# Performance work log

Measured on AMD Instinct MI355X. Metric: run time of the kernel, lower is better.

## Reference

```python
import jax, jax.numpy as jnp
from jax import lax
import numpy as np

VOCAB, EMB = 50000, 300
HID, NCLS = 100, 20
BATCH, SEQ = 128, 512
P_DROP = 0.5


def setup_inputs() -> dict:
    key = jax.random.key(0)
    ks = jax.random.split(key, 8)
    s_e = 1.0 / np.sqrt(EMB)
    s_h = 1.0 / np.sqrt(HID)
    return {
        "inputs_batch": jax.random.randint(ks[0], (BATCH, SEQ), 0, VOCAB, dtype=jnp.int64)
        if jax.config.jax_enable_x64 else jax.random.randint(ks[0], (BATCH, SEQ), 0, VOCAB, dtype=jnp.int32),
        "emb_table": jax.random.normal(ks[1], (VOCAB, EMB), dtype=jnp.float32),
        # GRUCell params (torch layout): gates order [r, z, n]
        "w_ih": jax.random.uniform(ks[2], (3 * HID, EMB), jnp.float32, -s_h, s_h),
        "w_hh": jax.random.uniform(ks[3], (3 * HID, HID), jnp.float32, -s_h, s_h),
        "b_ih": jax.random.uniform(ks[4], (3 * HID,), jnp.float32, -s_h, s_h),
        "b_hh": jax.random.uniform(ks[5], (3 * HID,), jnp.float32, -s_h, s_h),
        "w_lin": jax.random.uniform(ks[6], (NCLS, HID), jnp.float32, -s_h, s_h),
        "b_lin": jax.random.uniform(ks[7], (NCLS,), jnp.float32, -s_h, s_h),
    }


def reference(inputs_batch, emb_table, w_ih, w_hh, b_ih, b_hh, w_lin, b_lin):
    B, S = inputs_batch.shape
    H = w_hh.shape[1]
    keep = 1.0 - P_DROP
    dk1, dk2 = jax.random.split(jax.random.key(42))

    z_embed = emb_table[inputs_batch]                       # [B, S, E]
    m1 = jax.random.bernoulli(dk1, keep, z_embed.shape)     # dropout1 mask
    z_embed = jnp.where(m1, z_embed / keep, 0.0)
    x_seq = jnp.swapaxes(z_embed, 0, 1)                     # [S, B, E]
    m2 = jax.random.bernoulli(dk2, keep, (S, B, H))         # per-step dropout2 masks

    def step(h, inp):
        x, m = inp
        gi = x @ w_ih.T + b_ih                              # [B, 3H]
        gh = h @ w_hh.T + b_hh
        i_r, i_z, i_n = jnp.split(gi, 3, axis=-1)
        h_r, h_z, h_n = jnp.split(gh, 3, axis=-1)
        r = jax.nn.sigmoid(i_r + h_r)
        zg = jax.nn.sigmoid(i_z + h_z)
        n = jnp.tanh(i_n + r * h_n)
        h_new = (1.0 - zg) * n + zg * h
        h_d = jnp.where(m, h_new / keep, 0.0)
        y = jax.nn.log_softmax(h_d @ w_lin.T + b_lin, axis=1)  # [B, C]
        return h_new, y

    h0 = jnp.zeros((B, H), dtype=x_seq.dtype)
    _, ys = lax.scan(step, h0, (x_seq, m2))                 # ys: [S, B, C]
    return jnp.transpose(ys, (1, 2, 0))                     # [B, C, S]
```

## Files before the change

### kernel.cpp

```cpp
#include <hip/hip_runtime.h>
#include <hip/hip_bf16.h>
#include <cstdint>

#define BATCH 128
#define SEQ   512
#define EMB   300
#define HID   100
#define G3    300
#define NCLS  20
#define NROWS (SEQ * BATCH)

#define M1_WORDS 614400
#define M2_WORDS 204800

typedef __attribute__((ext_vector_type(4))) float f32x4;
typedef __attribute__((ext_vector_type(8))) short s16x8;
typedef __fp16 h16x2 __attribute__((ext_vector_type(2)));

__host__ __device__ __forceinline__ void threefry2x32(uint32_t k0, uint32_t k1,
                                                      uint32_t x0, uint32_t x1,
                                                      uint32_t* o0, uint32_t* o1) {
  uint32_t ks2 = k0 ^ k1 ^ 0x1BD11BDAu;
  x0 += k0; x1 += k1;
#define TFR(r) { x0 += x1; x1 = (x1 << (r)) | (x1 >> (32 - (r))); x1 ^= x0; }
  TFR(13) TFR(15) TFR(26) TFR(6)  x0 += k1;  x1 += ks2 + 1u;
  TFR(17) TFR(29) TFR(16) TFR(24) x0 += ks2; x1 += k0 + 2u;
  TFR(13) TFR(15) TFR(26) TFR(6)  x0 += k0;  x1 += k1 + 3u;
  TFR(17) TFR(29) TFR(16) TFR(24) x0 += k1;  x1 += ks2 + 4u;
  TFR(13) TFR(15) TFR(26) TFR(6)  x0 += ks2; x1 += k0 + 5u;
#undef TFR
  *o0 = x0; *o1 = x1;
}

__device__ __forceinline__ uint32_t rand_bits32(uint32_t ka, uint32_t kb, uint32_t flat) {
  uint32_t a, b;
  threefry2x32(ka, kb, 0u, flat, &a, &b);
  return a ^ b;
}

__device__ __forceinline__ short f2bf(float f) {
  union { float f; uint32_t u; } c; c.f = f;
  uint32_t u = c.u;
  return (short)((u + 0x7FFFu + ((u >> 16) & 1u)) >> 16);
}

__device__ __forceinline__ void bar_lds() {
  __asm__ __volatile__("s_waitcnt lgkmcnt(0)" ::: "memory");
  __builtin_amdgcn_s_barrier();
  __asm__ __volatile__("" ::: "memory");
}

__global__ __launch_bounds__(256) void k_mask(uint32_t* __restrict__ M1w,
                                              uint32_t* __restrict__ M2w,
                                              uint32_t k1a, uint32_t k1b,
                                              uint32_t k2a, uint32_t k2b) {
  const int i = blockIdx.x * 256 + threadIdx.x;
  uint32_t ka, kb, base;
  uint32_t* dst;
  if (i < M1_WORDS) { ka = k1a; kb = k1b; base = (uint32_t)i * 32u; dst = M1w + i; }
  else { ka = k2a; kb = k2b; base = (uint32_t)(i - M1_WORDS) * 32u; dst = M2w + (i - M1_WORDS); }
  uint32_t w = 0u;
#pragma unroll
  for (int j = 0; j < 32; ++j) {
    uint32_t bits = rand_bits32(ka, kb, base + (uint32_t)j);
    w |= ((~bits) >> 31) << j;
  }
  *dst = w;
}

__global__ __launch_bounds__(256) void k_prepw(const float* __restrict__ w_ih,
                                               short* __restrict__ Wb) {
  int i8 = (blockIdx.x * 256 + threadIdx.x) * 8;
  if (i8 >= 304 * 320) return;
  short o[8];
#pragma unroll
  for (int j = 0; j < 8; ++j) {
    int pos = i8 + j;
    int n = pos / 320, k = pos - (pos / 320) * 320;
    float v = (n < 300 && k < 300) ? w_ih[(size_t)n * EMB + k] : 0.f;
    o[j] = f2bf(v);
  }
  *(s16x8*)(Wb + i8) = *(s16x8*)o;
}

__global__ __launch_bounds__(512) void k_gi7(const int* __restrict__ inputs,
                                             const float* __restrict__ emb,
                                             const short* __restrict__ Wb,
                                             const float* __restrict__ b_ih,
                                             const uint32_t* __restrict__ M1w,
                                             float* __restrict__ GI) {
  __shared__ short As[128 * 40];
  __shared__ short Bs[304 * 40];
  __shared__ int idxs[128];
  const int t = threadIdx.x;
  const int s = blockIdx.x;
  const int lane = t & 63, wave = t >> 6;
  const int wr = wave & 1;
  const int wc = wave >> 1;
  const int ml = lane & 15, quad = lane >> 4;
  const int arow = t >> 2;
  const int akq = t & 3;

  if (t < 128) idxs[t] = inputs[t * SEQ + s];
  __syncthreads();

  const int nfr = (wc < 3) ? 5 : 4;
  f32x4 acc[4][5];
#pragma unroll
  for (int i = 0; i < 4; ++i)
#pragma unroll
    for (int j = 0; j < 5; ++j) acc[i][j] = (f32x4){0.f, 0.f, 0.f, 0.f};

  const int myidx = idxs[arow];

  for (int c = 0; c < 10; ++c) {
    const int e0 = c * 32 + akq * 8;
    float xa[8];
#pragma unroll
    for (int j = 0; j < 8; ++j) xa[j] = 0.f;
    if (e0 + 7 < 300) {
#pragma unroll
      for (int q4 = 0; q4 < 2; ++q4) {
        float4 v = *(const float4*)(emb + (size_t)myidx * EMB + e0 + q4 * 4);
        xa[q4 * 4 + 0] = v.x; xa[q4 * 4 + 1] = v.y; xa[q4 * 4 + 2] = v.z; xa[q4 * 4 + 3] = v.w;
      }
    } else if (e0 < 300) {
#pragma unroll
      for (int j = 0; j < 8; ++j) {
        int e = e0 + j;
        if (e < 300) xa[j] = emb[(size_t)myidx * EMB + e];
      }
    }
    uint32_t mb = 0;
    if (e0 < 300) {
      uint32_t base = (uint32_t)((arow * SEQ + s) * EMB + e0);
      uint64_t mw = (uint64_t)M1w[base >> 5] | ((uint64_t)M1w[(base >> 5) + 1] << 32);
      mb = (uint32_t)(mw >> (base & 31));
    }
    short sa[8];
#pragma unroll
    for (int j = 0; j < 8; ++j)
      sa[j] = f2bf(((mb >> j) & 1u) ? xa[j] * 2.f : 0.f);
    s16x8 bv0, bv1, bv2;
    {
      int i0 = t;
      bv0 = *(const s16x8*)(Wb + (size_t)(i0 >> 2) * 320 + c * 32 + (i0 & 3) * 8);
      int i1 = t + 512;
      bv1 = *(const s16x8*)(Wb + (size_t)(i1 >> 2) * 320 + c * 32 + (i1 & 3) * 8);
      if (t < 192) {
        int i2 = t + 1024;
        bv2 = *(const s16x8*)(Wb + (size_t)(i2 >> 2) * 320 + c * 32 + (i2 & 3) * 8);
      }
    }
    if (c > 0) __syncthreads();
    *(s16x8*)&As[arow * 40 + akq * 8] = *(s16x8*)&sa[0];
    {
      int i0 = t;       *(s16x8*)&Bs[(i0 >> 2) * 40 + (i0 & 3) * 8] = bv0;
      int i1 = t + 512; *(s16x8*)&Bs[(i1 >> 2) * 40 + (i1 & 3) * 8] = bv1;
      if (t < 192) { int i2 = t + 1024; *(s16x8*)&Bs[(i2 >> 2) * 40 + (i2 & 3) * 8] = bv2; }
    }
    __syncthreads();
    s16x8 af[4];
#pragma unroll
    for (int mt = 0; mt < 4; ++mt)
      af[mt] = *(const s16x8*)&As[(wr * 64 + mt * 16 + ml) * 40 + quad * 8];
#pragma unroll
    for (int j = 0; j < 5; ++j) {
      if (j < nfr) {
        int nt = wc + 4 * j;
        s16x8 bf = *(const s16x8*)&Bs[(nt * 16 + ml) * 40 + quad * 8];
#pragma unroll
        for (int mt = 0; mt < 4; ++mt)
          acc[mt][j] = __builtin_amdgcn_mfma_f32_16x16x32_bf16(af[mt], bf, acc[mt][j], 0, 0, 0);
      }
    }
  }

#pragma unroll
  for (int j = 0; j < 5; ++j) {
    if (j < nfr) {
      int n = (wc + 4 * j) * 16 + ml;
      if (n < 300) {
        float bias = b_ih[n];
#pragma unroll
        for (int mt = 0; mt < 4; ++mt) {
#pragma unroll
          for (int i = 0; i < 4; ++i) {
            int brow = wr * 64 + mt * 16 + quad * 4 + i;
            GI[(size_t)(s * BATCH + brow) * G3 + n] = acc[mt][j][i] + bias;
          }
        }
      }
    }
  }
}

__global__ __launch_bounds__(512, 1) void k_rnn10(const float* __restrict__ GI,
                                                  const float* __restrict__ w_hh,
                                                  const float* __restrict__ b_hh,
                                                  const uint8_t* __restrict__ M2,
                                                  float* __restrict__ Hd) {
  __shared__ float4 part[4][104];
  __shared__ __align__(8) float h_s[100];
  const int t = threadIdx.x, lane = t & 63, wave = t >> 6;
  const int q = wave >> 1, g = wave & 1;
  const int b = blockIdx.x;
  const int ulo = (lane < 36) ? lane : 35;
  const int u = g ? (64 + ulo) : lane;
  const bool dotstore = (g == 0) || (lane < 36);
  const int kplo = (q < 2) ? q * 13 : 26 + (q - 2) * 12;

  const float* rowR = w_hh + (size_t)u * HID;
  const float* rowZ = w_hh + (size_t)(u + 100) * HID;
  const float* rowN = w_hh + (size_t)(u + 200) * HID;
  const int o12 = (kplo + 12 < 50) ? 2 * (kplo + 12) : 96;
#define PK(row, off) __builtin_amdgcn_cvt_pkrtz((row)[off], (row)[(off) + 1])
  const h16x2 wr0 = PK(rowR, 2 * kplo + 0),  wr1 = PK(rowR, 2 * kplo + 2),
              wr2 = PK(rowR, 2 * kplo + 4),  wr3 = PK(rowR, 2 * kplo + 6),
              wr4 = PK(rowR, 2 * kplo + 8),  wr5 = PK(rowR, 2 * kplo + 10),
              wr6 = PK(rowR, 2 * kplo + 12), wr7 = PK(rowR, 2 * kplo + 14),
              wr8 = PK(rowR, 2 * kplo + 16), wr9 = PK(rowR, 2 * kplo + 18),
              wr10 = PK(rowR, 2 * kplo + 20), wr11 = PK(rowR, 2 * kplo + 22),
              wr12 = PK(rowR, o12);
  const h16x2 wz0 = PK(rowZ, 2 * kplo + 0),  wz1 = PK(rowZ, 2 * kplo + 2),
              wz2 = PK(rowZ, 2 * kplo + 4),  wz3 = PK(rowZ, 2 * kplo + 6),
              wz4 = PK(rowZ, 2 * kplo + 8),  wz5 = PK(rowZ, 2 * kplo + 10),
              wz6 = PK(rowZ, 2 * kplo + 12), wz7 = PK(rowZ, 2 * kplo + 14),
              wz8 = PK(rowZ, 2 * kplo + 16), wz9 = PK(rowZ, 2 * kplo + 18),
              wz10 = PK(rowZ, 2 * kplo + 20), wz11 = PK(rowZ, 2 * kplo + 22),
              wz12 = PK(rowZ, o12);
  const h16x2 wn0 = PK(rowN, 2 * kplo + 0),  wn1 = PK(rowN, 2 * kplo + 2),
              wn2 = PK(rowN, 2 * kplo + 4),  wn3 = PK(rowN, 2 * kplo + 6),
              wn4 = PK(rowN, 2 * kplo + 8),  wn5 = PK(rowN, 2 * kplo + 10),
              wn6 = PK(rowN, 2 * kplo + 12), wn7 = PK(rowN, 2 * kplo + 14),
              wn8 = PK(rowN, 2 * kplo + 16), wn9 = PK(rowN, 2 * kplo + 18),
              wn10 = PK(rowN, 2 * kplo + 20), wn11 = PK(rowN, 2 * kplo + 22),
              wn12 = PK(rowN, o12);
#undef PK

  const bool ew = (wave < 4) && (lane < 25);
  const int ue = wave * 25 + lane;
  float bR = 0.f, bZ = 0.f, bN = 0.f, gcR = 0.f, gcZ = 0.f, gcN = 0.f;
  uint8_t mc = 0;
  if (ew) {
    bR = b_hh[ue]; bZ = b_hh[100 + ue]; bN = b_hh[200 + ue];
    const float* g0 = GI + (size_t)b * G3;
    gcR = g0[ue]; gcZ = g0[100 + ue]; gcN = g0[200 + ue];
    mc = M2[(uint32_t)(b * HID + ue) >> 3];
  }

  if (t < 100) h_s[t] = 0.f;
  h16x2 hP = (h16x2){(__fp16)0.f, (__fp16)0.f};
  const int pl = (lane < 50) ? lane : 49;
  __syncthreads();

#define RLP(L) __builtin_bit_cast(h16x2, __builtin_amdgcn_readlane(__builtin_bit_cast(int, hP), (L)))
#define S1P(J, L) { h16x2 hh = RLP(L); \
    sR = __builtin_amdgcn_fdot2(wr##J, hh, sR, false); \
    sZ = __builtin_amdgcn_fdot2(wz##J, hh, sZ, false); \
    sN = __builtin_amdgcn_fdot2(wn##J, hh, sN, false); }
#define DOT12(L0) \
  S1P(0, (L0) + 0)  S1P(1, (L0) + 1)  S1P(2, (L0) + 2)  S1P(3, (L0) + 3)  \
  S1P(4, (L0) + 4)  S1P(5, (L0) + 5)  S1P(6, (L0) + 6)  S1P(7, (L0) + 7)  \
  S1P(8, (L0) + 8)  S1P(9, (L0) + 9)  S1P(10, (L0) + 10) S1P(11, (L0) + 11)
#define DOT13(L0) DOT12(L0) S1P(12, (L0) + 12)

  for (int s = 0; s < SEQ; ++s) {
    float gnR = 0.f, gnZ = 0.f, gnN = 0.f;
    uint8_t mn = 0;
    if (ew) {
      int sn = (s + 1 < SEQ) ? s + 1 : s;
      const float* gp = GI + (size_t)(sn * BATCH + b) * G3;
      gnR = gp[ue]; gnZ = gp[100 + ue]; gnN = gp[200 + ue];
      mn = M2[(uint32_t)((sn * BATCH + b) * HID + ue) >> 3];
    }

    float sR = 0.f, sZ = 0.f, sN = 0.f;
    switch (q) {
      case 0: { DOT13(0)  } break;
      case 1: { DOT13(13) } break;
      case 2: { DOT12(26) } break;
      case 3: { DOT12(38) } break;
    }
    if (dotstore) part[q][u] = make_float4(sR, sZ, sN, 0.f);
    bar_lds();

    if (wave < 4) {
      if (lane < 25) {
        float4 p0 = part[0][ue], p1 = part[1][ue], p2 = part[2][ue], p3 = part[3][ue];
        float hr = (p0.x + p1.x) + (p2.x + p3.x) + bR;
        float hz = (p0.y + p1.y) + (p2.y + p3.y) + bZ;
        float hn = (p0.z + p1.z) + (p2.z + p3.z) + bN;
        float r = 1.f / (1.f + __expf(-(gcR + hr)));
        float z = 1.f / (1.f + __expf(-(gcZ + hz)));
        float xn = gcN + r * hn;
        float e2 = __expf(2.f * fabsf(xn));
        float n = copysignf(1.f - 2.f / (e2 + 1.f), xn);
        float hprev = h_s[ue];
        float hnew = (1.f - z) * n + z * hprev;
        uint32_t fl = (uint32_t)((s * BATCH + b) * HID + ue);
        float hd = ((mc >> (fl & 7)) & 1) ? hnew * 2.f : 0.f;
        Hd[(size_t)(b * SEQ + s) * HID + ue] = hd;
        h_s[ue] = hnew;
      }
    }
    bar_lds();
    {
      float2 hp2 = *(const float2*)&h_s[2 * pl];
      hP = __builtin_amdgcn_cvt_pkrtz(hp2.x, hp2.y);
    }
    gcR = gnR; gcZ = gnZ; gcN = gnN; mc = mn;
  }
#undef DOT13
#undef DOT12
#undef S1P
#undef RLP
}

__global__ __launch_bounds__(64) void k_out(const float* __restrict__ Hd,
                                            const float* __restrict__ w_lin,
                                            const float* __restrict__ b_lin,
                                            float* __restrict__ out) {
  __shared__ float Wl[NCLS * HID];
  __shared__ float bl[NCLS];
  const int t = threadIdx.x;
  for (int i = t; i < NCLS * HID; i += 64) Wl[i] = w_lin[i];
  if (t < NCLS) bl[t] = b_lin[t];
  __syncthreads();

  const int r0 = (blockIdx.x * 64 + t) * 4;
  float acc[4][NCLS];
#pragma unroll
  for (int r = 0; r < 4; ++r)
#pragma unroll
    for (int c = 0; c < NCLS; ++c) acc[r][c] = bl[c];

  for (int k = 0; k < HID; k += 4) {
    float4 h0 = *(const float4*)(Hd + (size_t)(r0 + 0) * HID + k);
    float4 h1 = *(const float4*)(Hd + (size_t)(r0 + 1) * HID + k);
    float4 h2 = *(const float4*)(Hd + (size_t)(r0 + 2) * HID + k);
    float4 h3 = *(const float4*)(Hd + (size_t)(r0 + 3) * HID + k);
#pragma unroll
    for (int c = 0; c < NCLS; ++c) {
      float4 w4 = *(const float4*)&Wl[c * HID + k];
      acc[0][c] += h0.x * w4.x + h0.y * w4.y + h0.z * w4.z + h0.w * w4.w;
      acc[1][c] += h1.x * w4.x + h1.y * w4.y + h1.z * w4.z + h1.w * w4.w;
      acc[2][c] += h2.x * w4.x + h2.y * w4.y + h2.z * w4.z + h2.w * w4.w;
      acc[3][c] += h3.x * w4.x + h3.y * w4.y + h3.z * w4.z + h3.w * w4.w;
    }
  }

  float lse[4];
#pragma unroll
  for (int r = 0; r < 4; ++r) {
    float mx = acc[r][0];
#pragma unroll
    for (int c = 1; c < NCLS; ++c) mx = fmaxf(mx, acc[r][c]);
    float se = 0.f;
#pragma unroll
    for (int c = 0; c < NCLS; ++c) se += __expf(acc[r][c] - mx);
    lse[r] = mx + __logf(se);
  }
  const int b = r0 >> 9, s0 = r0 & 511;
#pragma unroll
  for (int c = 0; c < NCLS; ++c) {
    float4 o = make_float4(acc[0][c] - lse[0], acc[1][c] - lse[1],
                           acc[2][c] - lse[2], acc[3][c] - lse[3]);
    *(float4*)(out + (size_t)(b * NCLS + c) * SEQ + s0) = o;
  }
}

extern "C" void kernel_launch(void* const* d_in, const int* in_sizes, int n_in,
                              void* d_out, int out_size, void* d_ws, size_t ws_size,
                              hipStream_t stream) {
  const int*   inputs = (const int*)d_in[0];
  const float* emb    = (const float*)d_in[1];
  const float* w_ih   = (const float*)d_in[2];
  const float* w_hh   = (const float*)d_in[3];
  const float* b_ih   = (const float*)d_in[4];
  const float* b_hh   = (const float*)d_in[5];
  const float* w_lin  = (const float*)d_in[6];
  const float* b_lin  = (const float*)d_in[7];
  float* out = (float*)d_out;

  float* GI = (float*)d_ws;
  float* Hd = GI + (size_t)NROWS * G3;
  uint8_t* M1 = (uint8_t*)(Hd + (size_t)NROWS * HID);
  uint8_t* M2 = M1 + (size_t)M1_WORDS * 4;
  short* Wb = (short*)(M2 + (size_t)M2_WORDS * 4);

  uint32_t dk1a, dk1b, dk2a, dk2b;
  threefry2x32(0u, 42u, 0u, 0u, &dk1a, &dk1b);
  threefry2x32(0u, 42u, 0u, 1u, &dk2a, &dk2b);

  k_mask<<<(M1_WORDS + M2_WORDS) / 256, 256, 0, stream>>>(
      (uint32_t*)M1, (uint32_t*)M2, dk1a, dk1b, dk2a, dk2b);
  k_prepw<<<(304 * 320 / 8 + 255) / 256, 256, 0, stream>>>(w_ih, Wb);
  k_gi7<<<512, 512, 0, stream>>>(inputs, emb, Wb, b_ih, (const uint32_t*)M1, GI);
  k_rnn10<<<BATCH, 512, 0, stream>>>(GI, w_hh, b_hh, M2, Hd);
  k_out<<<256, 64, 0, stream>>>(Hd, w_lin, b_lin, out);
}
```

Measured before the change: 618.5 us.

## Restructure GRU recurrence to reduce K-splits via DPP and use one barrier per step

The recurrent kernel now maps four adjacent lanes to one hidden unit, each covering a quarter of the K dimension. Partial dot products are combined with DPP quad shuffles, so the LDS partial-sum buffer and the first barrier per step go away. Packed fp16 hidden state is exchanged through a double-buffered LDS array and read with vector loads instead of readlane, and hprev stays in a register. The trade-off is that every lane in the quad does redundant LDS reads of h and only one lane per quad computes the gates, which adds some divergence.

```diff
diff --git a/kernel.cpp b/kernel.cpp
--- a/kernel.cpp
+++ b/kernel.cpp
@@ -48,6 +48,11 @@
   __asm__ __volatile__("s_waitcnt lgkmcnt(0)" ::: "memory");
   __builtin_amdgcn_s_barrier();
   __asm__ __volatile__("" ::: "memory");
+}
+
+__device__ __forceinline__ float swz_xor4(float x) {
+  return __builtin_bit_cast(float,
+      __builtin_amdgcn_ds_swizzle(__builtin_bit_cast(int, x), 0x101F));
 }
 
 __global__ __launch_bounds__(256) void k_mask(uint32_t* __restrict__ M1w,
@@ -195,126 +200,106 @@
   }
 }
 
-__global__ __launch_bounds__(512, 1) void k_rnn10(const float* __restrict__ GI,
+__global__ __launch_bounds__(512, 1) void k_rnn11(const float* __restrict__ GI,
                                                   const float* __restrict__ w_hh,
                                                   const float* __restrict__ b_hh,
                                                   const uint8_t* __restrict__ M2,
                                                   float* __restrict__ Hd) {
-  __shared__ float4 part[4][104];
-  __shared__ __align__(8) float h_s[100];
-  const int t = threadIdx.x, lane = t & 63, wave = t >> 6;
-  const int q = wave >> 1, g = wave & 1;
-  const int b = blockIdx.x;
-  const int ulo = (lane < 36) ? lane : 35;
-  const int u = g ? (64 + ulo) : lane;
-  const bool dotstore = (g == 0) || (lane < 36);
-  const int kplo = (q < 2) ? q * 13 : 26 + (q - 2) * 12;
-
-  const float* rowR = w_hh + (size_t)u * HID;
-  const float* rowZ = w_hh + (size_t)(u + 100) * HID;
-  const float* rowN = w_hh + (size_t)(u + 200) * HID;
-  const int o12 = (kplo + 12 < 50) ? 2 * (kplo + 12) : 96;
-#define PK(row, off) __builtin_amdgcn_cvt_pkrtz((row)[off], (row)[(off) + 1])
-  const h16x2 wr0 = PK(rowR, 2 * kplo + 0),  wr1 = PK(rowR, 2 * kplo + 2),
-              wr2 = PK(rowR, 2 * kplo + 4),  wr3 = PK(rowR, 2 * kplo + 6),
-              wr4 = PK(rowR, 2 * kplo + 8),  wr5 = PK(rowR, 2 * kplo + 10),
-              wr6 = PK(rowR, 2 * kplo + 12), wr7 = PK(rowR, 2 * kplo + 14),
-              wr8 = PK(rowR, 2 * kplo + 16), wr9 = PK(rowR, 2 * kplo + 18),
-              wr10 = PK(rowR, 2 * kplo + 20), wr11 = PK(rowR, 2 * kplo + 22),
-              wr12 = PK(rowR, o12);
-  const h16x2 wz0 = PK(rowZ, 2 * kplo + 0),  wz1 = PK(rowZ, 2 * kplo + 2),
-              wz2 = PK(rowZ, 2 * kplo + 4),  wz3 = PK(rowZ, 2 * kplo + 6),
-              wz4 = PK(rowZ, 2 * kplo + 8),  wz5 = PK(rowZ, 2 * kplo + 10),
-              wz6 = PK(rowZ, 2 * kplo + 12), wz7 = PK(rowZ, 2 * kplo + 14),
-              wz8 = PK(rowZ, 2 * kplo + 16), wz9 = PK(rowZ, 2 * kplo + 18),
-              wz10 = PK(rowZ, 2 * kplo + 20), wz11 = PK(rowZ, 2 * kplo + 22),
-              wz12 = PK(rowZ, o12);
-  const h16x2 wn0 = PK(rowN, 2 * kplo + 0),  wn1 = PK(rowN, 2 * kplo + 2),
-              wn2 = PK(rowN, 2 * kplo + 4),  wn3 = PK(rowN, 2 * kplo + 6),
-              wn4 = PK(rowN, 2 * kplo + 8),  wn5 = PK(rowN, 2 * kplo + 10),
-              wn6 = PK(rowN, 2 * kplo + 12), wn7 = PK(rowN, 2 * kplo + 14),
-              wn8 = PK(rowN, 2 * kplo + 16), wn9 = PK(rowN, 2 * kplo + 18),
-              wn10 = PK(rowN, 2 * kplo + 20), wn11 = PK(rowN, 2 * kplo + 22),
-              wn12 = PK(rowN, o12);
-#undef PK
-
-  const bool ew = (wave < 4) && (lane < 25);
-  const int ue = wave * 25 + lane;
-  float bR = 0.f, bZ = 0.f, bN = 0.f, gcR = 0.f, gcZ = 0.f, gcN = 0.f;
+  __shared__ __align__(16) uint32_t hp_s[2][64];
+  const int t = threadIdx.x, b = blockIdx.x;
+  const int u = t >> 2, ks = t & 3;
+  const bool act = (u < 100);
+  const bool gate = act && (ks == 0);
+  const int uc = act ? u : 99;
+  const int kplo = (ks < 2) ? ks * 13 : 26 + (ks - 2) * 12;
+  const int np = (ks < 2) ? 13 : 12;
+
+  const float* rowR = w_hh + (size_t)uc * HID;
+  const float* rowZ = w_hh + (size_t)(uc + 100) * HID;
+  const float* rowN = w_hh + (size_t)(uc + 200) * HID;
+  const h16x2 z2 = (h16x2){(__fp16)0.f, (__fp16)0.f};
+  h16x2 wR[13], wZ[13], wN[13];
+#pragma unroll
+  for (int j = 0; j < 13; ++j) {
+    if (j < np) {
+      int o = 2 * (kplo + j);
+      wR[j] = __builtin_amdgcn_cvt_pkrtz(rowR[o], rowR[o + 1]);
+      wZ[j] = __builtin_amdgcn_cvt_pkrtz(rowZ[o], rowZ[o + 1]);
+      wN[j] = __builtin_amdgcn_cvt_pkrtz(rowN[o], rowN[o + 1]);
+    } else { wR[j] = z2; wZ[j] = z2; wN[j] = z2; }
+  }
+
+  float bR0 = 0.f, bZ0 = 0.f, bN0 = 0.f;
+  float gcR = 0.f, gcZ = 0.f, gcN = 0.f;
   uint8_t mc = 0;
-  if (ew) {
-    bR = b_hh[ue]; bZ = b_hh[100 + ue]; bN = b_hh[200 + ue];
+  if (gate) {
+    bR0 = b_hh[u]; bZ0 = b_hh[100 + u]; bN0 = b_hh[200 + u];
     const float* g0 = GI + (size_t)b * G3;
-    gcR = g0[ue]; gcZ = g0[100 + ue]; gcN = g0[200 + ue];
-    mc = M2[(uint32_t)(b * HID + ue) >> 3];
-  }
-
-  if (t < 100) h_s[t] = 0.f;
-  h16x2 hP = (h16x2){(__fp16)0.f, (__fp16)0.f};
-  const int pl = (lane < 50) ? lane : 49;
+    gcR = g0[u]; gcZ = g0[100 + u]; gcN = g0[200 + u];
+    mc = M2[(uint32_t)(b * HID + u) >> 3];
+  }
+  const int p = u >> 1;
+  const int sidx = (p < 13) ? 0 : (p < 26) ? 1 : (p < 38) ? 2 : 3;
+  const int spos = p - ((sidx < 2) ? sidx * 13 : 26 + (sidx - 2) * 12);
+  const int slot = sidx * 16 + spos;
+  const bool writer = gate && !(u & 1);
+
+  if (t < 128) ((uint32_t*)hp_s)[t] = 0u;
+  float hprev = 0.f;
   __syncthreads();
 
-#define RLP(L) __builtin_bit_cast(h16x2, __builtin_amdgcn_readlane(__builtin_bit_cast(int, hP), (L)))
-#define S1P(J, L) { h16x2 hh = RLP(L); \
-    sR = __builtin_amdgcn_fdot2(wr##J, hh, sR, false); \
-    sZ = __builtin_amdgcn_fdot2(wz##J, hh, sZ, false); \
-    sN = __builtin_amdgcn_fdot2(wn##J, hh, sN, false); }
-#define DOT12(L0) \
-  S1P(0, (L0) + 0)  S1P(1, (L0) + 1)  S1P(2, (L0) + 2)  S1P(3, (L0) + 3)  \
-  S1P(4, (L0) + 4)  S1P(5, (L0) + 5)  S1P(6, (L0) + 6)  S1P(7, (L0) + 7)  \
-  S1P(8, (L0) + 8)  S1P(9, (L0) + 9)  S1P(10, (L0) + 10) S1P(11, (L0) + 11)
-#define DOT13(L0) DOT12(L0) S1P(12, (L0) + 12)
-
+#define QPX(x, c) __builtin_bit_cast(float, __builtin_amdgcn_mov_dpp( \
+    __builtin_bit_cast(int, (x)), (c), 0xF, 0xF, true))
+#define DOT1(J, W) { h16x2 hh = __builtin_bit_cast(h16x2, (W)); \
+    sR = __builtin_amdgcn_fdot2(wR[J], hh, sR, false); \
+    sZ = __builtin_amdgcn_fdot2(wZ[J], hh, sZ, false); \
+    sN = __builtin_amdgcn_fdot2(wN[J], hh, sN, false); }
+
+#pragma unroll 2
   for (int s = 0; s < SEQ; ++s) {
     float gnR = 0.f, gnZ = 0.f, gnN = 0.f;
     uint8_t mn = 0;
-    if (ew) {
+    if (gate) {
       int sn = (s + 1 < SEQ) ? s + 1 : s;
       const float* gp = GI + (size_t)(sn * BATCH + b) * G3;
-      gnR = gp[ue]; gnZ = gp[100 + ue]; gnN = gp[200 + ue];
-      mn = M2[(uint32_t)((sn * BATCH + b) * HID + ue) >> 3];
-    }
-
-    float sR = 0.f, sZ = 0.f, sN = 0.f;
-    switch (q) {
-      case 0: { DOT13(0)  } break;
-      case 1: { DOT13(13) } break;
-      case 2: { DOT12(26) } break;
-      case 3: { DOT12(38) } break;
-    }
-    if (dotstore) part[q][u] = make_float4(sR, sZ, sN, 0.f);
-    bar_lds();
-
-    if (wave < 4) {
-      if (lane < 25) {
-        float4 p0 = part[0][ue], p1 = part[1][ue], p2 = part[2][ue], p3 = part[3][ue];
-        float hr = (p0.x + p1.x) + (p2.x + p3.x) + bR;
-        float hz = (p0.y + p1.y) + (p2.y + p3.y) + bZ;
-        float hn = (p0.z + p1.z) + (p2.z + p3.z) + bN;
-        float r = 1.f / (1.f + __expf(-(gcR + hr)));
-        float z = 1.f / (1.f + __expf(-(gcZ + hz)));
-        float xn = gcN + r * hn;
+      gnR = gp[u]; gnZ = gp[100 + u]; gnN = gp[200 + u];
+      mn = M2[(uint32_t)((sn * BATCH + b) * HID + u) >> 3];
+    }
+    if (act) {
+      float sR = bR0, sZ = bZ0, sN = bN0;
+      const uint32_t* hb = &hp_s[s & 1][0] + (ks << 4);
+      uint4 h0 = *(const uint4*)hb;
+      uint4 h1 = *(const uint4*)(hb + 4);
+      uint4 h2 = *(const uint4*)(hb + 8);
+      uint32_t h3 = hb[12];
+      DOT1(0, h0.x)  DOT1(1, h0.y)  DOT1(2, h0.z)  DOT1(3, h0.w)
+      DOT1(4, h1.x)  DOT1(5, h1.y)  DOT1(6, h1.z)  DOT1(7, h1.w)
+      DOT1(8, h2.x)  DOT1(9, h2.y)  DOT1(10, h2.z) DOT1(11, h2.w)
+      DOT1(12, h3)
+      sR += QPX(sR, 0xB1); sZ += QPX(sZ, 0xB1); sN += QPX(sN, 0xB1);
+      sR += QPX(sR, 0x4E); sZ += QPX(sZ, 0x4E); sN += QPX(sN, 0x4E);
+      if (gate) {
+        float r = 1.f / (1.f + __expf(-(gcR + sR)));
+        float z = 1.f / (1.f + __expf(-(gcZ + sZ)));
+        float xn = gcN + r * sN;
         float e2 = __expf(2.f * fabsf(xn));
         float n = copysignf(1.f - 2.f / (e2 + 1.f), xn);
-        float hprev = h_s[ue];
         float hnew = (1.f - z) * n + z * hprev;
-        uint32_t fl = (uint32_t)((s * BATCH + b) * HID + ue);
-        float hd = ((mc >> (fl & 7)) & 1) ? hnew * 2.f : 0.f;
-        Hd[(size_t)(b * SEQ + s) * HID + ue] = hd;
-        h_s[ue] = hnew;
-      }
-    }
+        hprev = hnew;
+        uint32_t fl = (uint32_t)((s * BATCH + b) * HID + u);
+        float hd = ((mc >> (fl & 7)) & 1u) ? hnew * 2.f : 0.f;
+        Hd[(size_t)(b * SEQ + s) * HID + u] = hd;
+        float hoth = swz_xor4(hnew);
+        if (writer)
+          hp_s[(s & 1) ^ 1][slot] =
+              __builtin_bit_cast(uint32_t, __builtin_amdgcn_cvt_pkrtz(hnew, hoth));
+      }
+    }
+    gcR = gnR; gcZ = gnZ; gcN = gnN; mc = mn;
     bar_lds();
-    {
-      float2 hp2 = *(const float2*)&h_s[2 * pl];
-      hP = __builtin_amdgcn_cvt_pkrtz(hp2.x, hp2.y);
-    }
-    gcR = gnR; gcZ = gnZ; gcN = gnN; mc = mn;
-  }
-#undef DOT13
-#undef DOT12
-#undef S1P
-#undef RLP
+  }
+#undef DOT1
+#undef QPX
 }
 
 __global__ __launch_bounds__(64) void k_out(const float* __restrict__ Hd,
@@ -397,6 +382,6 @@
       (uint32_t*)M1, (uint32_t*)M2, dk1a, dk1b, dk2a, dk2b);
   k_prepw<<<(304 * 320 / 8 + 255) / 256, 256, 0, stream>>>(w_ih, Wb);
   k_gi7<<<512, 512, 0, stream>>>(inputs, emb, Wb, b_ih, (const uint32_t*)M1, GI);
-  k_rnn10<<<BATCH, 512, 0, stream>>>(GI, w_hh, b_hh, M2, Hd);
+  k_rnn11<<<BATCH, 512, 0, stream>>>(GI, w_hh, b_hh, M2, Hd);
   k_out<<<256, 64, 0, stream>>>(Hd, w_lin, b_lin, out);
 }
```

Result: faster. 557.7 us (-9.8%).
